# Kernel tuning notes

Measured on AMD Instinct MI355X. Metric: run time of the kernel, lower is better.

Reference implementation:

```python
import jax, jax.numpy as jnp
import numpy as np

E = 800000
N = 50000
D = 128


def setup_inputs() -> dict:
    key = jax.random.key(0)
    k1, k2, k3, k4, k5 = jax.random.split(key, 5)
    messages = jax.random.normal(k1, (E, D), dtype=jnp.float32)
    dst_index = jax.random.randint(k2, (E,), 0, N, dtype=jnp.int32)
    h_prev = jax.random.normal(k3, (N, D), dtype=jnp.float32)
    # nn.Linear(5*D, D): weight [D, 5*D], bias [D]
    bound = 1.0 / np.sqrt(5 * D)
    W = jax.random.uniform(k4, (D, 5 * D), minval=-bound, maxval=bound, dtype=jnp.float32)
    b = jax.random.uniform(k5, (D,), minval=-bound, maxval=bound, dtype=jnp.float32)
    return {"messages": messages, "dst_index": dst_index, "h_prev": h_prev, "W": W, "b": b}


def reference(messages, dst_index, h_prev, W, b):
    n = h_prev.shape[0]
    ones = jnp.ones((messages.shape[0],), dtype=messages.dtype)
    count = jax.ops.segment_sum(ones, dst_index, num_segments=n)[:, None]       # [N,1]
    count_clamped = jnp.maximum(count, 1.0)
    sum_msg = jax.ops.segment_sum(messages, dst_index, num_segments=n)          # [N,D]
    mean_msg = sum_msg / count_clamped
    has_edge = count > 0
    # torch_scatter fills empty segments with 0 for max/min; segment_max/min give +/-inf
    max_msg = jnp.where(has_edge, jax.ops.segment_max(messages, dst_index, num_segments=n), 0.0)
    min_msg = jnp.where(has_edge, jax.ops.segment_min(messages, dst_index, num_segments=n), 0.0)
    sum_sq = jax.ops.segment_sum(messages * messages, dst_index, num_segments=n)
    mean_sq = sum_sq / count_clamped
    var = jnp.maximum(mean_sq - mean_msg * mean_msg, 1e-6)
    std_msg = jnp.sqrt(var)
    agg_feat = jnp.concatenate([mean_msg, max_msg, min_msg, std_msg, h_prev], axis=-1)  # [N,5D]
    return agg_feat @ W.T + b
```

## Files before the change

kernel.cpp:

```cpp
#include <hip/hip_runtime.h>
#include <hip/hip_bf16.h>
#include <cstdint>
#include <cstddef>

typedef unsigned short u16;
typedef unsigned int u32;
typedef __attribute__((ext_vector_type(8))) short short8;
typedef __attribute__((ext_vector_type(4))) float f32x4;

#define D_FEAT 128
#define CAP 64
#define NPB 32
#define ASTR 520

__global__ void zero_ints_kernel(int* __restrict__ a, int n) {
    int i = blockIdx.x * blockDim.x + threadIdx.x;
    int stride = gridDim.x * blockDim.x;
    for (; i < n; i += stride) a[i] = 0;
}

__global__ void wcvt_kernel(const float* __restrict__ W, u16* __restrict__ Wb, int n4) {
    int i = blockIdx.x * blockDim.x + threadIdx.x;
    if (i >= n4) return;
    float4 v = reinterpret_cast<const float4*>(W)[i];
    u16 o[4];
    float vv[4] = {v.x, v.y, v.z, v.w};
    #pragma unroll
    for (int t = 0; t < 4; ++t) {
        __hip_bfloat16 h = __float2bfloat16(vv[t]);
        o[t] = *reinterpret_cast<u16*>(&h);
    }
    reinterpret_cast<ushort2*>(Wb)[2 * i]     = make_ushort2(o[0], o[1]);
    reinterpret_cast<ushort2*>(Wb)[2 * i + 1] = make_ushort2(o[2], o[3]);
}

__device__ __forceinline__ u32 packbf16(float a, float b) {
    __hip_bfloat16 ha = __float2bfloat16(a);
    __hip_bfloat16 hb = __float2bfloat16(b);
    return (u32)*reinterpret_cast<u16*>(&ha) | ((u32)*reinterpret_cast<u16*>(&hb) << 16);
}

__global__ void scatter_kernel(const int* __restrict__ dst, int* __restrict__ cursor,
                               int* __restrict__ slots, int E) {
    int i = blockIdx.x * blockDim.x + threadIdx.x;
    int stride = gridDim.x * blockDim.x;
    for (; i < E; i += stride) {
        int d = dst[i];
        int p = atomicAdd(&cursor[d], 1);
        if (p < CAP) slots[(size_t)d * CAP + p] = i;
    }
}

__device__ __forceinline__ void upd(f32x4& s, f32x4& q, f32x4& mx, f32x4& mn, f32x4 v) {
    s += v;
    q += v * v;
    #pragma unroll
    for (int j = 0; j < 4; ++j) {
        mx[j] = fmaxf(mx[j], v[j]);
        mn[j] = fminf(mn[j], v[j]);
    }
}

__global__ __launch_bounds__(256) void fused_agg_gemm(
    const float* __restrict__ messages,
    const float* __restrict__ h_prev,
    const int* __restrict__ slots,
    const int* __restrict__ cursor,
    const u16* __restrict__ Wb,
    const float* __restrict__ bias,
    float* __restrict__ out,
    int N) {
    __shared__ __align__(16) u16 st[NPB * ASTR];

    const int wave = threadIdx.x >> 6;
    const int lane = threadIdx.x & 63;
    const int q = lane >> 4;
    const int ql = lane & 15;
    const int nb = blockIdx.x * NPB;

    #pragma unroll
    for (int t = 0; t < NPB / 16; ++t) {
        const int nd = nb + wave * (NPB / 4) + t * 4 + q;
        const bool ndok = nd < N;
        const int cntT = ndok ? cursor[nd] : 0;
        const int m = cntT < CAP ? cntT : CAP;
        const int* sl = slots + (size_t)nd * CAP;

        f32x4 s0 = {0.f, 0.f, 0.f, 0.f}, s1 = {0.f, 0.f, 0.f, 0.f};
        f32x4 q0 = {0.f, 0.f, 0.f, 0.f}, q1 = {0.f, 0.f, 0.f, 0.f};
        f32x4 mx0 = {-INFINITY, -INFINITY, -INFINITY, -INFINITY};
        f32x4 mx1 = mx0;
        f32x4 mn0 = {INFINITY, INFINITY, INFINITY, INFINITY};
        f32x4 mn1 = mn0;

        for (int k0 = 0; k0 < m; k0 += 16) {
            int mk = m - k0; if (mk > 16) mk = 16;
            int eid = (k0 + ql < m) ? sl[k0 + ql] : 0;
            int r = 0;
            for (; r + 4 <= mk; r += 4) {
                int e0 = __shfl(eid, 16 * q + r + 0, 64);
                int e1 = __shfl(eid, 16 * q + r + 1, 64);
                int e2 = __shfl(eid, 16 * q + r + 2, 64);
                int e3 = __shfl(eid, 16 * q + r + 3, 64);
                const float* p0 = messages + (size_t)e0 * D_FEAT + 8 * ql;
                const float* p1 = messages + (size_t)e1 * D_FEAT + 8 * ql;
                const float* p2 = messages + (size_t)e2 * D_FEAT + 8 * ql;
                const float* p3 = messages + (size_t)e3 * D_FEAT + 8 * ql;
                f32x4 a0 = *reinterpret_cast<const f32x4*>(p0);
                f32x4 b0 = *reinterpret_cast<const f32x4*>(p0 + 4);
                f32x4 a1 = *reinterpret_cast<const f32x4*>(p1);
                f32x4 b1 = *reinterpret_cast<const f32x4*>(p1 + 4);
                f32x4 a2 = *reinterpret_cast<const f32x4*>(p2);
                f32x4 b2 = *reinterpret_cast<const f32x4*>(p2 + 4);
                f32x4 a3 = *reinterpret_cast<const f32x4*>(p3);
                f32x4 b3 = *reinterpret_cast<const f32x4*>(p3 + 4);
                upd(s0, q0, mx0, mn0, a0); upd(s1, q1, mx1, mn1, b0);
                upd(s0, q0, mx0, mn0, a1); upd(s1, q1, mx1, mn1, b1);
                upd(s0, q0, mx0, mn0, a2); upd(s1, q1, mx1, mn1, b2);
                upd(s0, q0, mx0, mn0, a3); upd(s1, q1, mx1, mn1, b3);
            }
            for (; r < mk; ++r) {
                int e = __shfl(eid, 16 * q + r, 64);
                const float* p = messages + (size_t)e * D_FEAT + 8 * ql;
                f32x4 a = *reinterpret_cast<const f32x4*>(p);
                f32x4 b = *reinterpret_cast<const f32x4*>(p + 4);
                upd(s0, q0, mx0, mn0, a); upd(s1, q1, mx1, mn1, b);
            }
        }

        float inv = 1.0f / fmaxf((float)cntT, 1.0f);
        f32x4 meA = s0 * inv, meB = s1 * inv;
        f32x4 vA = q0 * inv - meA * meA;
        f32x4 vB = q1 * inv - meB * meB;
        f32x4 sdA, sdB;
        #pragma unroll
        for (int j = 0; j < 4; ++j) {
            sdA[j] = sqrtf(fmaxf(vA[j], 1e-6f));
            sdB[j] = sqrtf(fmaxf(vB[j], 1e-6f));
        }
        if (cntT == 0) {
            mx0 = (f32x4){0.f, 0.f, 0.f, 0.f}; mx1 = mx0;
            mn0 = mx0; mn1 = mx0;
        }

        if (ndok) {
            u32* ag = reinterpret_cast<u32*>(st + (size_t)(nd - nb) * ASTR);
            const int wi = 4 * ql;
            ag[  0 + wi + 0] = packbf16(meA[0], meA[1]);
            ag[  0 + wi + 1] = packbf16(meA[2], meA[3]);
            ag[  0 + wi + 2] = packbf16(meB[0], meB[1]);
            ag[  0 + wi + 3] = packbf16(meB[2], meB[3]);
            ag[ 64 + wi + 0] = packbf16(mx0[0], mx0[1]);
            ag[ 64 + wi + 1] = packbf16(mx0[2], mx0[3]);
            ag[ 64 + wi + 2] = packbf16(mx1[0], mx1[1]);
            ag[ 64 + wi + 3] = packbf16(mx1[2], mx1[3]);
            ag[128 + wi + 0] = packbf16(mn0[0], mn0[1]);
            ag[128 + wi + 1] = packbf16(mn0[2], mn0[3]);
            ag[128 + wi + 2] = packbf16(mn1[0], mn1[1]);
            ag[128 + wi + 3] = packbf16(mn1[2], mn1[3]);
            ag[192 + wi + 0] = packbf16(sdA[0], sdA[1]);
            ag[192 + wi + 1] = packbf16(sdA[2], sdA[3]);
            ag[192 + wi + 2] = packbf16(sdB[0], sdB[1]);
            ag[192 + wi + 3] = packbf16(sdB[2], sdB[3]);
        }
    }
    __syncthreads();

    const int rt = (wave >> 1) * 16;
    const int c0 = (wave & 1) * 64;
    const int lr = lane & 15;
    const int kg = lane >> 4;

    const u16* aL = st + (size_t)(rt + lr) * ASTR + kg * 8;
    const int rowA = nb + rt + lr;
    const bool okA = rowA < N;
    const float* hp = h_prev + (size_t)rowA * D_FEAT + kg * 8;
    const u16* bp = Wb + (size_t)(c0 + lr) * 640 + kg * 8;

    f32x4 acc[4];
    #pragma unroll
    for (int ct = 0; ct < 4; ++ct) acc[ct] = (f32x4){0.f, 0.f, 0.f, 0.f};

    #pragma unroll 4
    for (int k0 = 0; k0 < 512; k0 += 32) {
        short8 a = *reinterpret_cast<const short8*>(aL + k0);
        #pragma unroll
        for (int ct = 0; ct < 4; ++ct) {
            short8 b = *reinterpret_cast<const short8*>(bp + (size_t)(ct * 16) * 640 + k0);
            acc[ct] = __builtin_amdgcn_mfma_f32_16x16x32_bf16(a, b, acc[ct], 0, 0, 0);
        }
    }

    auto cvt8 = [](const float* p) -> short8 {
        float4 x = *reinterpret_cast<const float4*>(p);
        float4 y = *reinterpret_cast<const float4*>(p + 4);
        float v[8] = {x.x, x.y, x.z, x.w, y.x, y.y, y.z, y.w};
        short8 r;
        #pragma unroll
        for (int t = 0; t < 8; ++t) {
            __hip_bfloat16 h = __float2bfloat16(v[t]);
            r[t] = *reinterpret_cast<short*>(&h);
        }
        return r;
    };
    #pragma unroll
    for (int kh = 0; kh < 128; kh += 32) {
        short8 a = {};
        if (okA) a = cvt8(hp + kh);
        #pragma unroll
        for (int ct = 0; ct < 4; ++ct) {
            short8 b = *reinterpret_cast<const short8*>(bp + (size_t)(ct * 16) * 640 + 512 + kh);
            acc[ct] = __builtin_amdgcn_mfma_f32_16x16x32_bf16(a, b, acc[ct], 0, 0, 0);
        }
    }

    #pragma unroll
    for (int ct = 0; ct < 4; ++ct) {
        int col = c0 + ct * 16 + lr;
        float bv = bias[col];
        #pragma unroll
        for (int j = 0; j < 4; ++j) {
            int row = nb + rt + kg * 4 + j;
            if (row < N) out[(size_t)row * D_FEAT + col] = acc[ct][j] + bv;
        }
    }
}

extern "C" void kernel_launch(void* const* d_in, const int* in_sizes, int n_in,
                              void* d_out, int out_size, void* d_ws, size_t ws_size,
                              hipStream_t stream) {
    const float* messages = (const float*)d_in[0];
    const int*   dst      = (const int*)d_in[1];
    const float* h_prev   = (const float*)d_in[2];
    const float* W        = (const float*)d_in[3];
    const float* bias     = (const float*)d_in[4];
    float* out = (float*)d_out;

    const int E = in_sizes[1];
    const int D = in_sizes[4];
    const int N = in_sizes[2] / D;
    const int WN = in_sizes[3];

    size_t off = 0;
    auto alloc = [&](size_t bytes) -> void* {
        void* p = (char*)d_ws + off;
        off += (bytes + 255) & ~(size_t)255;
        return p;
    };
    int* cursor = (int*)alloc((size_t)N * 4);
    int* slots  = (int*)alloc((size_t)N * CAP * 4);
    u16* Wb     = (u16*)alloc((size_t)WN * 2);
    (void)ws_size; (void)D;

    zero_ints_kernel<<<196, 256, 0, stream>>>(cursor, N);
    wcvt_kernel<<<(WN / 4 + 255) / 256, 256, 0, stream>>>(W, Wb, WN / 4);

    scatter_kernel<<<2048, 256, 0, stream>>>(dst, cursor, slots, E);

    fused_agg_gemm<<<(N + NPB - 1) / NPB, 256, 0, stream>>>(
        messages, h_prev, slots, cursor, Wb, bias, out, N);
}
```

Measured before the change: 221.6 us.

## Remap gather to half-wave per node with 16-edge batched loads

```diff
diff --git a/kernel.cpp b/kernel.cpp
--- a/kernel.cpp
+++ b/kernel.cpp
@@ -13,25 +13,27 @@
 #define NPB 32
 #define ASTR 520
 
-__global__ void zero_ints_kernel(int* __restrict__ a, int n) {
-    int i = blockIdx.x * blockDim.x + threadIdx.x;
-    int stride = gridDim.x * blockDim.x;
-    for (; i < n; i += stride) a[i] = 0;
-}
-
-__global__ void wcvt_kernel(const float* __restrict__ W, u16* __restrict__ Wb, int n4) {
-    int i = blockIdx.x * blockDim.x + threadIdx.x;
-    if (i >= n4) return;
-    float4 v = reinterpret_cast<const float4*>(W)[i];
-    u16 o[4];
-    float vv[4] = {v.x, v.y, v.z, v.w};
-    #pragma unroll
-    for (int t = 0; t < 4; ++t) {
-        __hip_bfloat16 h = __float2bfloat16(vv[t]);
-        o[t] = *reinterpret_cast<u16*>(&h);
-    }
-    reinterpret_cast<ushort2*>(Wb)[2 * i]     = make_ushort2(o[0], o[1]);
-    reinterpret_cast<ushort2*>(Wb)[2 * i + 1] = make_ushort2(o[2], o[3]);
+__global__ void prep_kernel(int* __restrict__ cursor, int n,
+                            const float* __restrict__ W, u16* __restrict__ Wb, int n4) {
+    const int b = blockIdx.x;
+    if (b < 196) {
+        int i = b * 256 + threadIdx.x;
+        if (i < n) cursor[i] = 0;
+    } else {
+        int i = (b - 196) * 256 + threadIdx.x;
+        if (i < n4) {
+            float4 v = reinterpret_cast<const float4*>(W)[i];
+            u16 o[4];
+            float vv[4] = {v.x, v.y, v.z, v.w};
+            #pragma unroll
+            for (int t = 0; t < 4; ++t) {
+                __hip_bfloat16 hh = __float2bfloat16(vv[t]);
+                o[t] = *reinterpret_cast<u16*>(&hh);
+            }
+            reinterpret_cast<ushort2*>(Wb)[2 * i]     = make_ushort2(o[0], o[1]);
+            reinterpret_cast<ushort2*>(Wb)[2 * i + 1] = make_ushort2(o[2], o[3]);
+        }
+    }
 }
 
 __device__ __forceinline__ u32 packbf16(float a, float b) {
@@ -61,7 +63,7 @@
     }
 }
 
-__global__ __launch_bounds__(256) void fused_agg_gemm(
+__global__ __launch_bounds__(256, 4) void fused_agg_gemm(
     const float* __restrict__ messages,
     const float* __restrict__ h_prev,
     const int* __restrict__ slots,
@@ -74,94 +76,67 @@
 
     const int wave = threadIdx.x >> 6;
     const int lane = threadIdx.x & 63;
-    const int q = lane >> 4;
-    const int ql = lane & 15;
+    const int h = lane >> 5;
+    const int hl = lane & 31;
     const int nb = blockIdx.x * NPB;
 
-    #pragma unroll
-    for (int t = 0; t < NPB / 16; ++t) {
-        const int nd = nb + wave * (NPB / 4) + t * 4 + q;
+    #pragma unroll 1
+    for (int t = 0; t < 4; ++t) {
+        const int nd = nb + wave * 8 + t * 2 + h;
         const bool ndok = nd < N;
         const int cntT = ndok ? cursor[nd] : 0;
         const int m = cntT < CAP ? cntT : CAP;
         const int* sl = slots + (size_t)nd * CAP;
 
-        f32x4 s0 = {0.f, 0.f, 0.f, 0.f}, s1 = {0.f, 0.f, 0.f, 0.f};
-        f32x4 q0 = {0.f, 0.f, 0.f, 0.f}, q1 = {0.f, 0.f, 0.f, 0.f};
-        f32x4 mx0 = {-INFINITY, -INFINITY, -INFINITY, -INFINITY};
-        f32x4 mx1 = mx0;
-        f32x4 mn0 = {INFINITY, INFINITY, INFINITY, INFINITY};
-        f32x4 mn1 = mn0;
-
-        for (int k0 = 0; k0 < m; k0 += 16) {
-            int mk = m - k0; if (mk > 16) mk = 16;
-            int eid = (k0 + ql < m) ? sl[k0 + ql] : 0;
-            int r = 0;
-            for (; r + 4 <= mk; r += 4) {
-                int e0 = __shfl(eid, 16 * q + r + 0, 64);
-                int e1 = __shfl(eid, 16 * q + r + 1, 64);
-                int e2 = __shfl(eid, 16 * q + r + 2, 64);
-                int e3 = __shfl(eid, 16 * q + r + 3, 64);
-                const float* p0 = messages + (size_t)e0 * D_FEAT + 8 * ql;
-                const float* p1 = messages + (size_t)e1 * D_FEAT + 8 * ql;
-                const float* p2 = messages + (size_t)e2 * D_FEAT + 8 * ql;
-                const float* p3 = messages + (size_t)e3 * D_FEAT + 8 * ql;
-                f32x4 a0 = *reinterpret_cast<const f32x4*>(p0);
-                f32x4 b0 = *reinterpret_cast<const f32x4*>(p0 + 4);
-                f32x4 a1 = *reinterpret_cast<const f32x4*>(p1);
-                f32x4 b1 = *reinterpret_cast<const f32x4*>(p1 + 4);
-                f32x4 a2 = *reinterpret_cast<const f32x4*>(p2);
-                f32x4 b2 = *reinterpret_cast<const f32x4*>(p2 + 4);
-                f32x4 a3 = *reinterpret_cast<const f32x4*>(p3);
-                f32x4 b3 = *reinterpret_cast<const f32x4*>(p3 + 4);
-                upd(s0, q0, mx0, mn0, a0); upd(s1, q1, mx1, mn1, b0);
-                upd(s0, q0, mx0, mn0, a1); upd(s1, q1, mx1, mn1, b1);
-                upd(s0, q0, mx0, mn0, a2); upd(s1, q1, mx1, mn1, b2);
-                upd(s0, q0, mx0, mn0, a3); upd(s1, q1, mx1, mn1, b3);
+        f32x4 s = {0.f, 0.f, 0.f, 0.f}, qq = {0.f, 0.f, 0.f, 0.f};
+        f32x4 mx = {-INFINITY, -INFINITY, -INFINITY, -INFINITY};
+        f32x4 mn = {INFINITY, INFINITY, INFINITY, INFINITY};
+
+        int eidA = (hl < m) ? sl[hl] : 0;
+        int eidB = (32 + hl < m) ? sl[32 + hl] : 0;
+
+        const int mo = __shfl_xor(m, 32, 64);
+        const int mmax = m > mo ? m : mo;
+
+        for (int k0 = 0; k0 < mmax; k0 += 16) {
+            const int src = (k0 & 32) ? eidB : eidA;
+            const int base = 32 * h + (k0 & 16);
+            int lim = m - 1 - k0; lim = lim < 0 ? 0 : lim;
+
+            int e[16];
+            #pragma unroll
+            for (int r = 0; r < 16; ++r) {
+                int rr = r < lim ? r : lim;
+                e[r] = __shfl(src, base + rr, 64);
             }
-            for (; r < mk; ++r) {
-                int e = __shfl(eid, 16 * q + r, 64);
-                const float* p = messages + (size_t)e * D_FEAT + 8 * ql;
-                f32x4 a = *reinterpret_cast<const f32x4*>(p);
-                f32x4 b = *reinterpret_cast<const f32x4*>(p + 4);
-                upd(s0, q0, mx0, mn0, a); upd(s1, q1, mx1, mn1, b);
-            }
+            f32x4 v[16];
+            #pragma unroll
+            for (int r = 0; r < 16; ++r)
+                v[r] = *reinterpret_cast<const f32x4*>(
+                    messages + (size_t)e[r] * D_FEAT + 4 * hl);
+            #pragma unroll
+            for (int r = 0; r < 16; ++r)
+                if (k0 + r < m) upd(s, qq, mx, mn, v[r]);
         }
 
         float inv = 1.0f / fmaxf((float)cntT, 1.0f);
-        f32x4 meA = s0 * inv, meB = s1 * inv;
-        f32x4 vA = q0 * inv - meA * meA;
-        f32x4 vB = q1 * inv - meB * meB;
-        f32x4 sdA, sdB;
-        #pragma unroll
-        for (int j = 0; j < 4; ++j) {
-            sdA[j] = sqrtf(fmaxf(vA[j], 1e-6f));
-            sdB[j] = sqrtf(fmaxf(vB[j], 1e-6f));
-        }
+        f32x4 me = s * inv;
+        f32x4 var = qq * inv - me * me;
+        f32x4 sd;
+        #pragma unroll
+        for (int j = 0; j < 4; ++j) sd[j] = sqrtf(fmaxf(var[j], 1e-6f));
         if (cntT == 0) {
-            mx0 = (f32x4){0.f, 0.f, 0.f, 0.f}; mx1 = mx0;
-            mn0 = mx0; mn1 = mx0;
+            mx = (f32x4){0.f, 0.f, 0.f, 0.f};
+            mn = (f32x4){0.f, 0.f, 0.f, 0.f};
         }
 
         if (ndok) {
             u32* ag = reinterpret_cast<u32*>(st + (size_t)(nd - nb) * ASTR);
-            const int wi = 4 * ql;
-            ag[  0 + wi + 0] = packbf16(meA[0], meA[1]);
-            ag[  0 + wi + 1] = packbf16(meA[2], meA[3]);
-            ag[  0 + wi + 2] = packbf16(meB[0], meB[1]);
-            ag[  0 + wi + 3] = packbf16(meB[2], meB[3]);
-            ag[ 64 + wi + 0] = packbf16(mx0[0], mx0[1]);
-            ag[ 64 + wi + 1] = packbf16(mx0[2], mx0[3]);
-            ag[ 64 + wi + 2] = packbf16(mx1[0], mx1[1]);
-            ag[ 64 + wi + 3] = packbf16(mx1[2], mx1[3]);
-            ag[128 + wi + 0] = packbf16(mn0[0], mn0[1]);
-            ag[128 + wi + 1] = packbf16(mn0[2], mn0[3]);
-            ag[128 + wi + 2] = packbf16(mn1[0], mn1[1]);
-            ag[128 + wi + 3] = packbf16(mn1[2], mn1[3]);
-            ag[192 + wi + 0] = packbf16(sdA[0], sdA[1]);
-            ag[192 + wi + 1] = packbf16(sdA[2], sdA[3]);
-            ag[192 + wi + 2] = packbf16(sdB[0], sdB[1]);
-            ag[192 + wi + 3] = packbf16(sdB[2], sdB[3]);
+            const int wi = 2 * hl;
+            ag[  0 + wi] = packbf16(me[0], me[1]);  ag[  0 + wi + 1] = packbf16(me[2], me[3]);
+            ag[ 64 + wi] = packbf16(mx[0], mx[1]);  ag[ 64 + wi + 1] = packbf16(mx[2], mx[3]);
+            ag[128 + wi] = packbf16(mn[0], mn[1]);  ag[128 + wi + 1] = packbf16(mn[2], mn[3]);
+            ag[192 + wi] = packbf16(sd[0], sd[1]);  ag[192 + wi + 1] = packbf16(sd[2], sd[3]);
         }
     }
     __syncthreads();
@@ -198,8 +173,8 @@
         short8 r;
         #pragma unroll
         for (int t = 0; t < 8; ++t) {
-            __hip_bfloat16 h = __float2bfloat16(v[t]);
-            r[t] = *reinterpret_cast<short*>(&h);
+            __hip_bfloat16 hh = __float2bfloat16(v[t]);
+            r[t] = *reinterpret_cast<short*>(&hh);
         }
         return r;
     };
@@ -252,8 +227,9 @@
     u16* Wb     = (u16*)alloc((size_t)WN * 2);
     (void)ws_size; (void)D;
 
-    zero_ints_kernel<<<196, 256, 0, stream>>>(cursor, N);
-    wcvt_kernel<<<(WN / 4 + 255) / 256, 256, 0, stream>>>(W, Wb, WN / 4);
+    const int zb = (N + 255) / 256;
+    const int wb = (WN / 4 + 255) / 256;
+    prep_kernel<<<zb + wb, 256, 0, stream>>>(cursor, N, W, Wb, WN / 4);
 
     scatter_kernel<<<2048, 256, 0, stream>>>(dst, cursor, slots, E);
 
```

After: 219.3 us. Within noise of the previous version (-1.0%).
